# Performance work log

Hardware: AMD Instinct MI355X
Metric: run time of the kernel (lower is better)

Reference implementation:

```python
import jax, jax.numpy as jnp
import numpy as np

DT = 0.1
TAU = 1.0

def setup_inputs() -> dict:
    key = jax.random.key(0)
    ks = jax.random.split(key, 5)
    B, T, IN_C, N, R, OUT_C = 64, 1024, 16, 512, 16, 8
    return {
        "Batch_Input": jax.random.normal(ks[0], (B, T, IN_C), dtype=jnp.float32),
        "In_w": jax.random.normal(ks[1], (N, IN_C), dtype=jnp.float32),
        "V_w": jax.random.normal(ks[2], (R, N), dtype=jnp.float32) / np.float32(np.sqrt(N)),
        "U_w": jax.random.normal(ks[3], (N, R), dtype=jnp.float32) / np.float32(np.sqrt(R)),
        "Out_w": jax.random.normal(ks[4], (OUT_C, N), dtype=jnp.float32),
        "hidden_0": jnp.zeros((N,), dtype=jnp.float32),
    }

def reference(Batch_Input, In_w, V_w, U_w, Out_w, hidden_0):
    # Eval-mode forward (no noise injection), faithful to the torch math.
    B, T, _ = Batch_Input.shape
    a = DT / TAU  # leak integration coefficient
    # Input projection: [B, T, in_C] @ [in_C, N] -> [B, T, N]
    Inp = jnp.einsum('bti,ni->btn', Batch_Input, In_w)
    h0 = jnp.broadcast_to(hidden_0, (B, hidden_0.shape[0]))
    Inp_t = jnp.transpose(Inp, (1, 0, 2))  # [T, B, N] for scan

    def step(h, inp_t):
        phi = jnp.tanh(h)                       # act_func = Tanh
        low = jnp.einsum('bn,rn->br', phi, V_w)  # V: N -> r
        rec = jnp.einsum('br,nr->bn', low, U_w)  # U: r -> N
        h_new = (1.0 - a) * h + a * (rec + inp_t)
        return h_new, h_new

    _, hs = jax.lax.scan(step, h0, Inp_t)       # hs: [T, B, N]
    hidden_t = jnp.transpose(hs, (1, 0, 2))      # [B, T, N]
    out = jnp.einsum('btn,on->bto', jnp.tanh(hidden_t), Out_w)  # [B, T, out_C]
    return hidden_t, out
```

## Files before the change

### kernel.cpp

```cpp
#include <hip/hip_runtime.h>

#define BATCH 64
#define TT    1024
#define INC   16
#define NN    512
#define RNK   16
#define OUTC  8

#define A_COEF 0.1f

__device__ __forceinline__ float fast_tanh(float x) {
    float e = __expf(2.0f * x);
    return 1.0f - __fdividef(2.0f, e + 1.0f);
}

__device__ __forceinline__ void lgkm_barrier() {
    asm volatile("s_waitcnt lgkmcnt(0)\n\ts_barrier" ::: "memory");
}

template<int CTRL>
__device__ __forceinline__ float dpp_add(float x) {
    int y = __builtin_amdgcn_update_dpp(0, __float_as_int(x), CTRL, 0xF, 0xF, true);
    return x + __int_as_float(y);
}

__device__ __forceinline__ float half_wave_sum(float x) {
    x = dpp_add<0x111>(x);
    x = dpp_add<0x112>(x);
    x = dpp_add<0x114>(x);
    x = dpp_add<0x118>(x);
    x = dpp_add<0x142>(x);
    return x;
}

__device__ __forceinline__ float wave_sum(float x) {
    x = half_wave_sum(x);
    x = dpp_add<0x143>(x);
    return x;
}

__global__ __launch_bounds__(512, 1) void scan_kernel(
    const float* __restrict__ x,
    const float* __restrict__ In_w,
    const float* __restrict__ V_w,
    const float* __restrict__ U_w,
    const float* __restrict__ Out_w,
    const float* __restrict__ h0,
    float* __restrict__ hidden,
    float* __restrict__ out)
{
    const int b   = blockIdx.x;
    const int tid = threadIdx.x;
    const int rr  = tid >> 5;
    const int g   = tid & 31;
    const int ow  = tid >> 6;
    const int p   = tid & 63;

    __shared__ __align__(16) float xs[TT * INC];
    __shared__ __align__(16) float phi_s[NN];
    __shared__ __align__(16) float low_s[RNK];

    {
        const float4* src = (const float4*)(x + (size_t)b * TT * INC);
        float4* dst = (float4*)xs;
        #pragma unroll
        for (int c = 0; c < 8; ++c)
            dst[c * 512 + tid] = src[c * 512 + tid];
    }

    float Ur[RNK];
    #pragma unroll
    for (int r = 0; r < RNK; ++r) Ur[r] = U_w[tid * RNK + r];

    float Wr[INC];
    #pragma unroll
    for (int i = 0; i < INC; ++i) Wr[i] = In_w[tid * INC + i];

    float Vr[16];
    #pragma unroll
    for (int k = 0; k < 4; ++k)
        #pragma unroll
        for (int j = 0; j < 4; ++j)
            Vr[k * 4 + j] = V_w[rr * NN + k * 128 + g * 4 + j];

    float Owr[8];
    #pragma unroll
    for (int j = 0; j < 8; ++j) Owr[j] = Out_w[ow * NN + p * 8 + j];

    float h = h0[tid];

    __syncthreads();

    float* hb = hidden + (size_t)b * TT * NN;
    float* ob = out + (size_t)b * TT * OUTC;

    float4 xv0, xv1, xv2, xv3;
    {
        const float4* xp = (const float4*)xs;
        xv0 = xp[0]; xv1 = xp[1]; xv2 = xp[2]; xv3 = xp[3];
    }

    for (int t = 0; t < TT; ++t) {
        float phi = fast_tanh(h);
        phi_s[tid] = phi;

        float ia = Wr[0] * xv0.x;
        float ib = Wr[1] * xv0.y;
        float ic = Wr[2] * xv0.z;
        float id = Wr[3] * xv0.w;
        ia = fmaf(Wr[4],  xv1.x, ia);
        ib = fmaf(Wr[5],  xv1.y, ib);
        ic = fmaf(Wr[6],  xv1.z, ic);
        id = fmaf(Wr[7],  xv1.w, id);
        ia = fmaf(Wr[8],  xv2.x, ia);
        ib = fmaf(Wr[9],  xv2.y, ib);
        ic = fmaf(Wr[10], xv2.z, ic);
        id = fmaf(Wr[11], xv2.w, id);
        ia = fmaf(Wr[12], xv3.x, ia);
        ib = fmaf(Wr[13], xv3.y, ib);
        ic = fmaf(Wr[14], xv3.z, ic);
        id = fmaf(Wr[15], xv3.w, id);
        float inp = (ia + ib) + (ic + id);

        lgkm_barrier();

        float p0 = 0.f, p1 = 0.f, p2 = 0.f, p3 = 0.f;
        #pragma unroll
        for (int k = 0; k < 4; ++k) {
            float4 ph = *(const float4*)&phi_s[k * 128 + g * 4];
            p0 = fmaf(Vr[k * 4 + 0], ph.x, p0);
            p1 = fmaf(Vr[k * 4 + 1], ph.y, p1);
            p2 = fmaf(Vr[k * 4 + 2], ph.z, p2);
            p3 = fmaf(Vr[k * 4 + 3], ph.w, p3);
        }
        float partial = (p0 + p1) + (p2 + p3);
        partial = half_wave_sum(partial);
        if (g == 31) low_s[rr] = partial;

        {
            int tn = (t + 1 < TT) ? t + 1 : t;
            const float4* xp = (const float4*)(xs + tn * INC);
            xv0 = xp[0]; xv1 = xp[1]; xv2 = xp[2]; xv3 = xp[3];
        }

        float4 q0 = *(const float4*)&phi_s[p * 8];
        float4 q1 = *(const float4*)&phi_s[p * 8 + 4];
        float oa = Owr[0] * q0.x;
        float obb = Owr[1] * q0.y;
        float oc = Owr[2] * q0.z;
        float od = Owr[3] * q0.w;
        oa  = fmaf(Owr[4], q1.x, oa);
        obb = fmaf(Owr[5], q1.y, obb);
        oc  = fmaf(Owr[6], q1.z, oc);
        od  = fmaf(Owr[7], q1.w, od);
        float osum = (oa + obb) + (oc + od);
        osum = wave_sum(osum);
        if (t > 0 && p == 63)
            ob[(t - 1) * OUTC + ow] = osum;

        lgkm_barrier();

        float4 l0 = *(const float4*)&low_s[0];
        float4 l1 = *(const float4*)&low_s[4];
        float4 l2 = *(const float4*)&low_s[8];
        float4 l3 = *(const float4*)&low_s[12];
        float ra = Ur[0] * l0.x;
        float rb = Ur[1] * l0.y;
        float rc = Ur[2] * l0.z;
        float rd = Ur[3] * l0.w;
        ra = fmaf(Ur[4],  l1.x, ra);
        rb = fmaf(Ur[5],  l1.y, rb);
        rc = fmaf(Ur[6],  l1.z, rc);
        rd = fmaf(Ur[7],  l1.w, rd);
        ra = fmaf(Ur[8],  l2.x, ra);
        rb = fmaf(Ur[9],  l2.y, rb);
        rc = fmaf(Ur[10], l2.z, rc);
        rd = fmaf(Ur[11], l2.w, rd);
        ra = fmaf(Ur[12], l3.x, ra);
        rb = fmaf(Ur[13], l3.y, rb);
        rc = fmaf(Ur[14], l3.z, rc);
        rd = fmaf(Ur[15], l3.w, rd);
        float rec = (ra + rb) + (rc + rd);

        h = fmaf(A_COEF, (rec + inp) - h, h);
        hb[t * NN + tid] = h;
    }

    float phi = fast_tanh(h);
    phi_s[tid] = phi;
    lgkm_barrier();
    {
        float4 q0 = *(const float4*)&phi_s[p * 8];
        float4 q1 = *(const float4*)&phi_s[p * 8 + 4];
        float oa = Owr[0] * q0.x;
        float obb = Owr[1] * q0.y;
        float oc = Owr[2] * q0.z;
        float od = Owr[3] * q0.w;
        oa  = fmaf(Owr[4], q1.x, oa);
        obb = fmaf(Owr[5], q1.y, obb);
        oc  = fmaf(Owr[6], q1.z, oc);
        od  = fmaf(Owr[7], q1.w, od);
        float osum = (oa + obb) + (oc + od);
        osum = wave_sum(osum);
        if (p == 63)
            ob[(TT - 1) * OUTC + ow] = osum;
    }
}

extern "C" void kernel_launch(void* const* d_in, const int* in_sizes, int n_in,
                              void* d_out, int out_size, void* d_ws, size_t ws_size,
                              hipStream_t stream) {
    const float* x    = (const float*)d_in[0];
    const float* In_w = (const float*)d_in[1];
    const float* V_w  = (const float*)d_in[2];
    const float* U_w  = (const float*)d_in[3];
    const float* Ow   = (const float*)d_in[4];
    const float* h0   = (const float*)d_in[5];

    float* hidden = (float*)d_out;
    float* out    = hidden + (size_t)BATCH * TT * NN;

    scan_kernel<<<BATCH, 512, 0, stream>>>(x, In_w, V_w, U_w, Ow, h0, hidden, out);
}
```

Baseline: 811.7 us.

## Split output projection into separate kernel and pack two batches per block

Removes the per-step tanh·Out_w projection from the serial recurrence and moves it to a second kernel that re-reads the hidden states and computes outputs in parallel. The scan kernel now runs two batch rows per 1024-thread block, each half with its own shared buffers, and reads x straight from global memory instead of staging it in LDS. The goal is a shorter per-step critical path in the latency-bound scan. The cost is an extra full pass over the 128 MB hidden tensor and a 1024-thread barrier that now synchronizes two independent batches.

```diff
diff --git a/kernel.cpp b/kernel.cpp
--- a/kernel.cpp
+++ b/kernel.cpp
@@ -39,34 +39,22 @@
     return x;
 }
 
-__global__ __launch_bounds__(512, 1) void scan_kernel(
+__global__ __launch_bounds__(1024) void scan_kernel(
     const float* __restrict__ x,
     const float* __restrict__ In_w,
     const float* __restrict__ V_w,
     const float* __restrict__ U_w,
-    const float* __restrict__ Out_w,
     const float* __restrict__ h0,
-    float* __restrict__ hidden,
-    float* __restrict__ out)
+    float* __restrict__ hidden)
 {
-    const int b   = blockIdx.x;
-    const int tid = threadIdx.x;
-    const int rr  = tid >> 5;
-    const int g   = tid & 31;
-    const int ow  = tid >> 6;
-    const int p   = tid & 63;
-
-    __shared__ __align__(16) float xs[TT * INC];
-    __shared__ __align__(16) float phi_s[NN];
-    __shared__ __align__(16) float low_s[RNK];
-
-    {
-        const float4* src = (const float4*)(x + (size_t)b * TT * INC);
-        float4* dst = (float4*)xs;
-        #pragma unroll
-        for (int c = 0; c < 8; ++c)
-            dst[c * 512 + tid] = src[c * 512 + tid];
-    }
+    const int half = threadIdx.x >> 9;
+    const int tid  = threadIdx.x & 511;
+    const int b    = (blockIdx.x << 1) | half;
+    const int rr   = tid >> 5;
+    const int g    = tid & 31;
+
+    __shared__ __align__(16) float phi_s[2][NN];
+    __shared__ __align__(16) float low_s[2][RNK];
 
     float Ur[RNK];
     #pragma unroll
@@ -83,26 +71,20 @@
         for (int j = 0; j < 4; ++j)
             Vr[k * 4 + j] = V_w[rr * NN + k * 128 + g * 4 + j];
 
-    float Owr[8];
-    #pragma unroll
-    for (int j = 0; j < 8; ++j) Owr[j] = Out_w[ow * NN + p * 8 + j];
-
     float h = h0[tid];
 
-    __syncthreads();
-
+    const float* xb = x + (size_t)b * TT * INC;
     float* hb = hidden + (size_t)b * TT * NN;
-    float* ob = out + (size_t)b * TT * OUTC;
 
     float4 xv0, xv1, xv2, xv3;
     {
-        const float4* xp = (const float4*)xs;
+        const float4* xp = (const float4*)xb;
         xv0 = xp[0]; xv1 = xp[1]; xv2 = xp[2]; xv3 = xp[3];
     }
 
     for (int t = 0; t < TT; ++t) {
         float phi = fast_tanh(h);
-        phi_s[tid] = phi;
+        phi_s[half][tid] = phi;
 
         float ia = Wr[0] * xv0.x;
         float ib = Wr[1] * xv0.y;
@@ -127,7 +109,7 @@
         float p0 = 0.f, p1 = 0.f, p2 = 0.f, p3 = 0.f;
         #pragma unroll
         for (int k = 0; k < 4; ++k) {
-            float4 ph = *(const float4*)&phi_s[k * 128 + g * 4];
+            float4 ph = *(const float4*)&phi_s[half][k * 128 + g * 4];
             p0 = fmaf(Vr[k * 4 + 0], ph.x, p0);
             p1 = fmaf(Vr[k * 4 + 1], ph.y, p1);
             p2 = fmaf(Vr[k * 4 + 2], ph.z, p2);
@@ -135,35 +117,20 @@
         }
         float partial = (p0 + p1) + (p2 + p3);
         partial = half_wave_sum(partial);
-        if (g == 31) low_s[rr] = partial;
+        if (g == 31) low_s[half][rr] = partial;
 
         {
             int tn = (t + 1 < TT) ? t + 1 : t;
-            const float4* xp = (const float4*)(xs + tn * INC);
+            const float4* xp = (const float4*)(xb + tn * INC);
             xv0 = xp[0]; xv1 = xp[1]; xv2 = xp[2]; xv3 = xp[3];
         }
 
-        float4 q0 = *(const float4*)&phi_s[p * 8];
-        float4 q1 = *(const float4*)&phi_s[p * 8 + 4];
-        float oa = Owr[0] * q0.x;
-        float obb = Owr[1] * q0.y;
-        float oc = Owr[2] * q0.z;
-        float od = Owr[3] * q0.w;
-        oa  = fmaf(Owr[4], q1.x, oa);
-        obb = fmaf(Owr[5], q1.y, obb);
-        oc  = fmaf(Owr[6], q1.z, oc);
-        od  = fmaf(Owr[7], q1.w, od);
-        float osum = (oa + obb) + (oc + od);
-        osum = wave_sum(osum);
-        if (t > 0 && p == 63)
-            ob[(t - 1) * OUTC + ow] = osum;
-
         lgkm_barrier();
 
-        float4 l0 = *(const float4*)&low_s[0];
-        float4 l1 = *(const float4*)&low_s[4];
-        float4 l2 = *(const float4*)&low_s[8];
-        float4 l3 = *(const float4*)&low_s[12];
+        float4 l0 = *(const float4*)&low_s[half][0];
+        float4 l1 = *(const float4*)&low_s[half][4];
+        float4 l2 = *(const float4*)&low_s[half][8];
+        float4 l3 = *(const float4*)&low_s[half][12];
         float ra = Ur[0] * l0.x;
         float rb = Ur[1] * l0.y;
         float rc = Ur[2] * l0.z;
@@ -185,25 +152,50 @@
         h = fmaf(A_COEF, (rec + inp) - h, h);
         hb[t * NN + tid] = h;
     }
-
-    float phi = fast_tanh(h);
-    phi_s[tid] = phi;
-    lgkm_barrier();
-    {
-        float4 q0 = *(const float4*)&phi_s[p * 8];
-        float4 q1 = *(const float4*)&phi_s[p * 8 + 4];
-        float oa = Owr[0] * q0.x;
-        float obb = Owr[1] * q0.y;
-        float oc = Owr[2] * q0.z;
-        float od = Owr[3] * q0.w;
-        oa  = fmaf(Owr[4], q1.x, oa);
-        obb = fmaf(Owr[5], q1.y, obb);
-        oc  = fmaf(Owr[6], q1.z, oc);
-        od  = fmaf(Owr[7], q1.w, od);
-        float osum = (oa + obb) + (oc + od);
-        osum = wave_sum(osum);
-        if (p == 63)
-            ob[(TT - 1) * OUTC + ow] = osum;
+}
+
+__global__ __launch_bounds__(256) void out_kernel(
+    const float* __restrict__ hidden,
+    const float* __restrict__ Out_w,
+    float* __restrict__ out)
+{
+    const int wv = (blockIdx.x << 2) | (threadIdx.x >> 6);
+    const int p  = threadIdx.x & 63;
+    const int NW = gridDim.x << 2;
+
+    float Ow[OUTC][8];
+    #pragma unroll
+    for (int o = 0; o < OUTC; ++o) {
+        float4 w0 = *(const float4*)&Out_w[o * NN + p * 4];
+        float4 w1 = *(const float4*)&Out_w[o * NN + 256 + p * 4];
+        Ow[o][0] = w0.x; Ow[o][1] = w0.y; Ow[o][2] = w0.z; Ow[o][3] = w0.w;
+        Ow[o][4] = w1.x; Ow[o][5] = w1.y; Ow[o][6] = w1.z; Ow[o][7] = w1.w;
+    }
+
+    const int ROWS = BATCH * TT;
+    for (int r = wv; r < ROWS; r += NW) {
+        const float4* hp = (const float4*)(hidden + (size_t)r * NN);
+        float4 a = hp[p];
+        float4 c = hp[64 + p];
+        float ph[8];
+        ph[0] = fast_tanh(a.x); ph[1] = fast_tanh(a.y);
+        ph[2] = fast_tanh(a.z); ph[3] = fast_tanh(a.w);
+        ph[4] = fast_tanh(c.x); ph[5] = fast_tanh(c.y);
+        ph[6] = fast_tanh(c.z); ph[7] = fast_tanh(c.w);
+        #pragma unroll
+        for (int o = 0; o < OUTC; ++o) {
+            float sa = Ow[o][0] * ph[0];
+            float sb = Ow[o][1] * ph[1];
+            sa = fmaf(Ow[o][2], ph[2], sa);
+            sb = fmaf(Ow[o][3], ph[3], sb);
+            sa = fmaf(Ow[o][4], ph[4], sa);
+            sb = fmaf(Ow[o][5], ph[5], sb);
+            sa = fmaf(Ow[o][6], ph[6], sa);
+            sb = fmaf(Ow[o][7], ph[7], sb);
+            float s = sa + sb;
+            s = wave_sum(s);
+            if (p == 63) out[(size_t)r * OUTC + o] = s;
+        }
     }
 }
 
@@ -220,5 +212,6 @@
     float* hidden = (float*)d_out;
     float* out    = hidden + (size_t)BATCH * TT * NN;
 
-    scan_kernel<<<BATCH, 512, 0, stream>>>(x, In_w, V_w, U_w, Ow, h0, hidden, out);
-}
+    scan_kernel<<<BATCH / 2, 1024, 0, stream>>>(x, In_w, V_w, U_w, h0, hidden);
+    out_kernel<<<1024, 256, 0, stream>>>(hidden, Ow, out);
+}
```

After: 1.131 ms. 39.3% more time.
